# Kernel optimization log

Hardware: AMD Instinct MI355X
Metric: run time of the kernel (lower is better)

## Reference

```python
import jax, jax.numpy as jnp
import numpy as np

# ---- problem sizes ----
N_NEURONS = 1536
N_INPUTS = 768
BATCH = 32
T = 256
DT = 1.0  # ms per step
SURRGRAD_SCALE = 10.0

# ---- per-cell-type physiology (recurrent): 0=excitatory, 1=inhibitory ----
CELL_TAU_MEM = np.array([20.0, 10.0], np.float32)   # ms
CELL_THETA   = np.array([-50.0, -50.0], np.float32) # mV
CELL_URESET  = np.array([-65.0, -65.0], np.float32) # mV
CELL_EL      = np.array([-65.0, -65.0], np.float32) # mV
CELL_GL      = np.array([10.0, 10.0], np.float32)   # nS
CELL_TAUREF  = np.array([2.0, 1.0], np.float32)     # ms

# ---- synapse types: AMPA(pre=exc), NMDA(pre=exc), GABA_A(pre=inh) ----
SYN_CELL_ID   = np.array([0, 0, 1], np.int32)
SYN_TAU_RISE  = np.array([0.5, 2.0, 0.5], np.float32)
SYN_TAU_DECAY = np.array([2.0, 100.0, 5.0], np.float32)
SYN_EREV      = np.array([0.0, 0.0, -70.0], np.float32)
SYN_GBAR      = np.array([1.0, 0.5, 1.0], np.float32)

# ---- feedforward: single excitatory input type, single AMPA synapse ----
FF_TAU_RISE, FF_TAU_DECAY, FF_EREV, FF_GBAR = 0.5, 2.0, 0.0, 1.0


@jax.custom_vjp
def spike(v):
    # Heaviside spike with fast-sigmoid surrogate gradient
    return (v >= 0).astype(v.dtype)

def _spike_fwd(v):
    return spike(v), v

def _spike_bwd(v, g):
    return (g / (SURRGRAD_SCALE * jnp.abs(v) + 1.0) ** 2,)

spike.defvjp(_spike_fwd, _spike_bwd)


def setup_inputs() -> dict:
    key = jax.random.key(0)
    ks = jax.random.split(key, 6)
    input_spikes = (jax.random.uniform(ks[0], (BATCH, T, N_INPUTS)) < 0.05).astype(jnp.float32)
    weights = jax.random.normal(ks[1], (N_NEURONS, N_NEURONS), jnp.float32) * 0.05
    weights_FF = jax.random.normal(ks[2], (N_INPUTS, N_NEURONS), jnp.float32) * 0.05
    cell_type_indices = jax.random.randint(ks[3], (N_NEURONS,), 0, 2, jnp.int32)
    cell_type_indices_FF = jnp.zeros((N_INPUTS,), jnp.int32)
    scaling_factors = jax.random.uniform(ks[4], (2, 2), jnp.float32, 0.5, 1.5)
    scaling_factors_FF = jax.random.uniform(ks[5], (1, 2), jnp.float32, 0.5, 1.5)
    return {
        'input_spikes': input_spikes,
        'weights': weights,
        'weights_FF': weights_FF,
        'scaling_factors': scaling_factors,
        'scaling_factors_FF': scaling_factors_FF,
        'cell_type_indices': cell_type_indices,
        'cell_type_indices_FF': cell_type_indices_FF,
    }


def _simulate(input_spikes, weights, weights_FF, scaling_factors, scaling_factors_FF,
              cell_type_indices, cell_type_indices_FF):
    ct = cell_type_indices
    B = input_spikes.shape[0]

    # per-neuron physiology gathered by cell type
    tau_mem = jnp.asarray(CELL_TAU_MEM)[ct]
    theta = jnp.asarray(CELL_THETA)[ct]
    u_reset = jnp.asarray(CELL_URESET)[ct]
    e_l = jnp.asarray(CELL_EL)[ct]
    g_l = jnp.asarray(CELL_GL)[ct]
    ref_steps = jnp.asarray(CELL_TAUREF)[ct] / DT
    leak_coef = DT / (tau_mem * g_l)  # dt / C_m

    # effective weights: cell-type scaling + presynaptic synapse-type mask
    sf = scaling_factors[ct[:, None], ct[None, :]]            # (N, N)
    W = weights * sf
    pre_mask = (jnp.asarray(SYN_CELL_ID)[:, None] == ct[None, :]).astype(W.dtype)  # (S, N)
    Ws = W[None, :, :] * pre_mask[:, :, None]                  # (S, N, N)
    sfF = scaling_factors_FF[cell_type_indices_FF[:, None], ct[None, :]]
    WF = weights_FF * sfF                                      # (n_in, N)

    alpha_r = jnp.exp(-DT / jnp.asarray(SYN_TAU_RISE))[:, None, None]   # (S,1,1)
    alpha_d = jnp.exp(-DT / jnp.asarray(SYN_TAU_DECAY))[:, None, None]
    arF = jnp.exp(jnp.float32(-DT / FF_TAU_RISE))
    adF = jnp.exp(jnp.float32(-DT / FF_TAU_DECAY))
    gbar = jnp.asarray(SYN_GBAR)
    gbarE = jnp.asarray(SYN_GBAR * SYN_EREV)
    S = gbar.shape[0]

    U0 = jnp.broadcast_to(e_l, (B, N_NEURONS))
    carry0 = (U0,
              jnp.zeros((B, N_NEURONS), jnp.float32),       # previous spikes
              jnp.zeros((S, B, N_NEURONS), jnp.float32),    # x (rise)
              jnp.zeros((S, B, N_NEURONS), jnp.float32),    # g (decay)
              jnp.zeros((B, N_NEURONS), jnp.float32),       # x_FF
              jnp.zeros((B, N_NEURONS), jnp.float32),       # g_FF
              jnp.zeros((B, N_NEURONS), jnp.float32))       # refractory counter

    def step(carry, I_t):
        U, s_prev, x, g, xF, gF, ref = carry
        # dual-exponential conductance update per synapse type
        inp = jnp.einsum('bn,snm->sbm', s_prev, Ws)
        x = alpha_r * x + inp
        g = alpha_d * g + x
        xF = arF * xF + I_t @ WF
        gF = adF * gF + xF
        # conductance-based synaptic current: sum_s gbar_s * g_s * (E_s - U)
        gtot = jnp.einsum('s,sbn->bn', gbar, g) + FF_GBAR * gF
        gE = jnp.einsum('s,sbn->bn', gbarE, g) + (FF_GBAR * FF_EREV) * gF
        I_syn = gE - gtot * U
        # leaky membrane integration
        U_new = U + leak_coef * (g_l * (e_l - U) + I_syn)
        # refractory clamp
        in_ref = ref > 0
        U_new = jnp.where(in_ref, u_reset, U_new)
        ref = jnp.maximum(ref - 1.0, 0.0)
        # surrogate-gradient spike and reset
        s_new = spike(U_new - theta)
        U_out = jnp.where(s_new > 0, u_reset, U_new)
        ref = jnp.where(s_new > 0, ref_steps, ref)
        return (U_out, s_new, x, g, xF, gF, ref), (s_new, U_out)

    I_seq = jnp.transpose(input_spikes, (1, 0, 2))  # (T, B, n_in)
    _, (spk, volts) = jax.lax.scan(step, carry0, I_seq)
    return jnp.transpose(spk, (1, 0, 2)), jnp.transpose(volts, (1, 0, 2))


def reference(input_spikes, weights, weights_FF, scaling_factors, scaling_factors_FF,
              cell_type_indices, cell_type_indices_FF):
    return _simulate(input_spikes, weights, weights_FF, scaling_factors, scaling_factors_FF,
                     cell_type_indices, cell_type_indices_FF)
```

## Files before the change

kernel.cpp:

```cpp
#include <hip/hip_runtime.h>
#include <stdint.h>


__global__ __launch_bounds__(768) void snn_lif_kernel(
    const float* __restrict__ I,
    const float* __restrict__ W,
    const float* __restrict__ WF,
    const float* __restrict__ sf,
    const float* __restrict__ sfF,
    const int*   __restrict__ ct,
    float* __restrict__ out,
    uint64_t* __restrict__ recpub)
{
    const int tid = threadIdx.x;
    const int j   = blockIdx.x & 7;
    const int b   = blockIdx.x >> 3;
    const int wv  = tid >> 6;
    const int wl  = tid & 63;

    __shared__ float4   part0[2][12][48];
    __shared__ float4   part1[2][12][48];
    __shared__ float4   partF[2][12][48];
    __shared__ uint32_t ctm32_sh[48];

    for (int r = 0; r < 2; ++r) {
        int c = ct[r * 768 + tid];
        uint64_t bal = __ballot(c != 0);
        if (wl == 0) {
            ctm32_sh[r * 24 + wv * 2]     = (uint32_t)bal;
            ctm32_sh[r * 24 + wv * 2 + 1] = (uint32_t)(bal >> 32);
        }
    }
    __syncthreads();

    const int m = j * 192 + ((tid < 192) ? tid : 0);
    const int   myct = ct[m];
    const float s0m  = sf[myct];
    const float s1m  = sf[2 + myct];
    const float sFm  = sfF[myct];
    const float lc   = (myct == 0) ? (1.0f / 200.0f) : (1.0f / 100.0f);
    const float refsteps = (myct == 0) ? 2.0f : 1.0f;
    const float ar0 = expf(-1.0f / 0.5f),  ad0 = expf(-1.0f / 2.0f);
    const float ar1 = expf(-1.0f / 2.0f),  ad1 = expf(-1.0f / 100.0f);
    const float ar2 = expf(-1.0f / 0.5f),  ad2 = expf(-1.0f / 5.0f);
    const float arF = expf(-1.0f / 0.5f),  adF = expf(-1.0f / 2.0f);

    float U = -65.0f, refc = 0.0f;
    float x0 = 0, g0 = 0, x1 = 0, g1 = 0, x2 = 0, g2 = 0, xF = 0, gF = 0;

    const int  btbase  = b * 256;
    const bool gl      = (wl < 48);
    const uint32_t colbase = (uint32_t)(j * 192 + wl * 4);

    uint64_t fmask;
    {
        float iv = __builtin_nontemporal_load(
            &I[(uint32_t)btbase * 768u + (uint32_t)tid]);
        fmask = __ballot(iv > 0.5f);
    }

    for (int t = 0; t < 256; ++t) {
        float ivn = 0.0f;
        if (t < 255)
            ivn = __builtin_nontemporal_load(
                &I[(uint32_t)(btbase + t + 1) * 768u + (uint32_t)tid]);

        float4 a0 = make_float4(0.f, 0.f, 0.f, 0.f);
        float4 a1 = a0, aF = a0;

        {
            uint64_t mm = fmask;
            while (mm) {
                const int bit = __builtin_ctzll(mm);
                mm &= mm - 1;
                const uint32_t row = (uint32_t)(wv * 64 + bit);
                if (gl) {
                    const float4 w = *(const float4*)(WF + row * 1536u + colbase);
                    aF.x += w.x; aF.y += w.y; aF.z += w.z; aF.w += w.w;
                }
            }
        }

        if (t > 0) {
            uint32_t ready = 0;
            const uint32_t pbase = (uint32_t)(btbase + t - 1) * 48u + (uint32_t)(wv * 4);
            do {
                uint64_t pv = 0;
                if (wl < 4)
                    pv = __hip_atomic_load(&recpub[pbase + (uint32_t)wl],
                                           __ATOMIC_RELAXED, __HIP_MEMORY_SCOPE_AGENT);
                const uint32_t plo = (uint32_t)pv;
                const uint32_t phi = (uint32_t)(pv >> 32);
                #pragma unroll
                for (int k = 0; k < 4; ++k) {
                    if (ready & (1u << k)) continue;
                    const uint32_t tg = __builtin_amdgcn_readlane(phi, k);
                    if (tg != (uint32_t)t) continue;
                    ready |= 1u << k;
                    uint32_t bits = __builtin_amdgcn_readlane(plo, k);
                    const uint32_t word = (uint32_t)(wv * 4 + k);
                    const uint32_t cm = ctm32_sh[word];
                    while (bits) {
                        const int bit = __builtin_ctz(bits);
                        bits &= bits - 1;
                        const uint32_t row = word * 32u + (uint32_t)bit;
                        if (gl) {
                            const float4 w = *(const float4*)(W + row * 1536u + colbase);
                            if ((cm >> bit) & 1u) {
                                a1.x += w.x; a1.y += w.y; a1.z += w.z; a1.w += w.w;
                            } else {
                                a0.x += w.x; a0.y += w.y; a0.z += w.z; a0.w += w.w;
                            }
                        }
                    }
                }
            } while (ready != 0xFu);
        }

        const int buf = t & 1;
        if (gl) {
            part0[buf][wv][wl] = a0;
            part1[buf][wv][wl] = a1;
            partF[buf][wv][wl] = aF;
        }
        fmask = __ballot(ivn > 0.5f);
        __syncthreads();

        if (tid < 192) {
            const float* p0 = (const float*)&part0[buf][0][0];
            const float* p1 = (const float*)&part1[buf][0][0];
            const float* pF = (const float*)&partF[buf][0][0];
            float z0s = 0.f, z1s = 0.f, zFs = 0.f;
            #pragma unroll
            for (int k = 0; k < 12; ++k) {
                z0s += p0[k * 192 + tid];
                z1s += p1[k * 192 + tid];
                zFs += pF[k * 192 + tid];
            }
            z0s *= s0m; z1s *= s1m; zFs *= sFm;
            x0 = ar0 * x0 + z0s;  g0 = ad0 * g0 + x0;
            x1 = ar1 * x1 + z0s;  g1 = ad1 * g1 + x1;
            x2 = ar2 * x2 + z1s;  g2 = ad2 * g2 + x2;
            xF = arF * xF + zFs;  gF = adF * gF + xF;
            const float gtot = g0 + 0.5f * g1 + g2 + gF;
            const float gE   = -70.0f * g2;
            const float Isyn = gE - gtot * U;
            float Un = U + lc * (10.0f * (-65.0f - U) + Isyn);
            if (refc > 0.0f) Un = -65.0f;
            refc = fmaxf(refc - 1.0f, 0.0f);
            const bool s = (Un - (-50.0f)) >= 0.0f;
            const uint64_t bal = __ballot(s);
            if (wl == 0 || wl == 32) {
                const uint32_t half = (wl == 0) ? (uint32_t)bal : (uint32_t)(bal >> 32);
                const uint32_t word = (uint32_t)(j * 6 + wv * 2) + (wl == 32 ? 1u : 0u);
                const uint32_t widx = (uint32_t)(btbase + t) * 48u + word;
                const uint64_t v = ((uint64_t)(uint32_t)(t + 1) << 32) | half;
                __hip_atomic_store(&recpub[widx], v, __ATOMIC_RELAXED,
                                   __HIP_MEMORY_SCOPE_AGENT);
            }
            const float Uo = s ? -65.0f : Un;
            refc = s ? refsteps : refc;
            U = Uo;
            const uint32_t oidx = (uint32_t)(btbase + t) * 1536u + (uint32_t)m;
            __builtin_nontemporal_store(s ? 1.0f : 0.0f, &out[oidx]);
            __builtin_nontemporal_store(Uo, &out[12582912u + oidx]);
        }
    }
}

extern "C" void kernel_launch(void* const* d_in, const int* in_sizes, int n_in,
                              void* d_out, int out_size, void* d_ws, size_t ws_size,
                              hipStream_t stream) {
    const float* I   = (const float*)d_in[0];
    const float* W   = (const float*)d_in[1];
    const float* WF  = (const float*)d_in[2];
    const float* sf  = (const float*)d_in[3];
    const float* sfF = (const float*)d_in[4];
    const int*   ct  = (const int*)d_in[5];

    uint64_t* recpub = (uint64_t*)d_ws;

    snn_lif_kernel<<<dim3(256), dim3(768), 0, stream>>>(
        I, W, WF, sf, sfF, ct, (float*)d_out, recpub);
}
```

Before: 748.1 us.

## Overlap feedforward gather with recurrent wait and batch weight loads

Result: no change. 760.1 us (+1.6%).

```diff
diff --git a/kernel.cpp b/kernel.cpp
--- a/kernel.cpp
+++ b/kernel.cpp
@@ -1,6 +1,56 @@
 #include <hip/hip_runtime.h>
 #include <stdint.h>
 
+
+__device__ __forceinline__ uint64_t ld_g_sc0(const uint64_t* p) {
+    uint64_t v;
+    asm volatile("global_load_dwordx2 %0, %1, off sc0\n\t"
+                 "s_waitcnt vmcnt(0)"
+                 : "=v"(v) : "v"(p) : "memory");
+    return v;
+}
+
+__device__ __forceinline__ void st_g_sc0(uint64_t* p, uint64_t v) {
+    asm volatile("global_store_dwordx2 %0, %1, off sc0"
+                 :: "v"(p), "v"(v) : "memory");
+}
+
+__device__ __forceinline__ float4 ff_gather(const float* __restrict__ WF,
+                                            uint64_t mm, uint32_t rowbase,
+                                            uint32_t colbase) {
+    float4 acc = make_float4(0.f, 0.f, 0.f, 0.f);
+    while (mm) {
+        uint32_t q0 = 0, q1 = 0, q2 = 0, q3 = 0;
+        bool e1 = false, e2 = false, e3 = false;
+        { int bq = (int)__builtin_ctzll(mm); mm &= mm - 1; q0 = rowbase + (uint32_t)bq; }
+        if (mm) { int bq = (int)__builtin_ctzll(mm); mm &= mm - 1; q1 = rowbase + (uint32_t)bq; e1 = true; }
+        if (mm) { int bq = (int)__builtin_ctzll(mm); mm &= mm - 1; q2 = rowbase + (uint32_t)bq; e2 = true; }
+        if (mm) { int bq = (int)__builtin_ctzll(mm); mm &= mm - 1; q3 = rowbase + (uint32_t)bq; e3 = true; }
+        float4 u0, u1, u2, u3;
+        u0 = *(const float4*)(WF + q0 * 1536u + colbase);
+        if (e1) u1 = *(const float4*)(WF + q1 * 1536u + colbase);
+        if (e2) u2 = *(const float4*)(WF + q2 * 1536u + colbase);
+        if (e3) u3 = *(const float4*)(WF + q3 * 1536u + colbase);
+        acc.x += u0.x; acc.y += u0.y; acc.z += u0.z; acc.w += u0.w;
+        if (e1) { acc.x += u1.x; acc.y += u1.y; acc.z += u1.z; acc.w += u1.w; }
+        if (e2) { acc.x += u2.x; acc.y += u2.y; acc.z += u2.z; acc.w += u2.w; }
+        if (e3) { acc.x += u3.x; acc.y += u3.y; acc.z += u3.z; acc.w += u3.w; }
+    }
+    return acc;
+}
+
+#define POP_ROW(RV, CV, HV)                                                        \
+    {                                                                              \
+        HV = false;                                                                \
+        if (nb0)      { int _b = (int)__builtin_ctz(nb0); nb0 &= nb0 - 1;          \
+                        RV = wbase + (uint32_t)_b;        CV = (cm0 >> _b) & 1u; HV = true; } \
+        else if (nb1) { int _b = (int)__builtin_ctz(nb1); nb1 &= nb1 - 1;          \
+                        RV = wbase + 32u + (uint32_t)_b;  CV = (cm1 >> _b) & 1u; HV = true; } \
+        else if (nb2) { int _b = (int)__builtin_ctz(nb2); nb2 &= nb2 - 1;          \
+                        RV = wbase + 64u + (uint32_t)_b;  CV = (cm2 >> _b) & 1u; HV = true; } \
+        else if (nb3) { int _b = (int)__builtin_ctz(nb3); nb3 &= nb3 - 1;          \
+                        RV = wbase + 96u + (uint32_t)_b;  CV = (cm3 >> _b) & 1u; HV = true; } \
+    }
 
 __global__ __launch_bounds__(768) void snn_lif_kernel(
     const float* __restrict__ I,
@@ -10,13 +60,17 @@
     const float* __restrict__ sfF,
     const int*   __restrict__ ct,
     float* __restrict__ out,
-    uint64_t* __restrict__ recpub)
+    uint64_t* __restrict__ recpub,
+    uint64_t* __restrict__ recfast)
 {
+    __builtin_amdgcn_fence(__ATOMIC_ACQUIRE, "agent");
+
     const int tid = threadIdx.x;
-    const int j   = blockIdx.x & 7;
-    const int b   = blockIdx.x >> 3;
+    const int b   = blockIdx.x & 31;
+    const int j   = blockIdx.x >> 5;
     const int wv  = tid >> 6;
     const int wl  = tid & 63;
+    const bool havefast = (recfast != nullptr);
 
     __shared__ float4   part0[2][12][48];
     __shared__ float4   part1[2][12][48];
@@ -32,6 +86,11 @@
         }
     }
     __syncthreads();
+
+    const uint32_t cm0 = ctm32_sh[wv * 4 + 0];
+    const uint32_t cm1 = ctm32_sh[wv * 4 + 1];
+    const uint32_t cm2 = ctm32_sh[wv * 4 + 2];
+    const uint32_t cm3 = ctm32_sh[wv * 4 + 3];
 
     const int m = j * 192 + ((tid < 192) ? tid : 0);
     const int   myct = ct[m];
@@ -50,72 +109,84 @@
 
     const int  btbase  = b * 256;
     const bool gl      = (wl < 48);
-    const uint32_t colbase = (uint32_t)(j * 192 + wl * 4);
-
-    uint64_t fmask;
+    const uint32_t colbase = (uint32_t)(j * 192) + (uint32_t)((wl < 48 ? wl : 47) * 4);
+    const uint32_t wbase   = (uint32_t)(wv * 128);
+    const uint32_t ffbase  = (uint32_t)(wv * 64);
+
+    float4 aF;
     {
         float iv = __builtin_nontemporal_load(
             &I[(uint32_t)btbase * 768u + (uint32_t)tid]);
-        fmask = __ballot(iv > 0.5f);
+        uint64_t f0 = __ballot(iv > 0.5f);
+        aF = ff_gather(WF, f0, ffbase, colbase);
     }
 
     for (int t = 0; t < 256; ++t) {
+        float4 a0 = make_float4(0.f, 0.f, 0.f, 0.f);
+        float4 a1 = a0;
+
+        if (t > 0) {
+            uint32_t ready = 0;
+            const uint32_t pbase = (uint32_t)(btbase + t - 1) * 48u + (uint32_t)(wv * 4);
+            uint32_t nb0 = 0, nb1 = 0, nb2 = 0, nb3 = 0;
+            int it = 0;
+            do {
+                uint64_t pv = 0;
+                if (wl < 4) {
+                    if (havefast && ((it & 1) == 0))
+                        pv = ld_g_sc0(&recfast[pbase + (uint32_t)wl]);
+                    else
+                        pv = __hip_atomic_load(&recpub[pbase + (uint32_t)wl],
+                                               __ATOMIC_RELAXED, __HIP_MEMORY_SCOPE_AGENT);
+                }
+                ++it;
+                const uint32_t plo = (uint32_t)pv;
+                const uint32_t phi = (uint32_t)(pv >> 32);
+                if (!(ready & 1u) && (uint32_t)__builtin_amdgcn_readlane(phi, 0) == (uint32_t)t) {
+                    ready |= 1u; nb0 = (uint32_t)__builtin_amdgcn_readlane(plo, 0);
+                }
+                if (!(ready & 2u) && (uint32_t)__builtin_amdgcn_readlane(phi, 1) == (uint32_t)t) {
+                    ready |= 2u; nb1 = (uint32_t)__builtin_amdgcn_readlane(plo, 1);
+                }
+                if (!(ready & 4u) && (uint32_t)__builtin_amdgcn_readlane(phi, 2) == (uint32_t)t) {
+                    ready |= 4u; nb2 = (uint32_t)__builtin_amdgcn_readlane(plo, 2);
+                }
+                if (!(ready & 8u) && (uint32_t)__builtin_amdgcn_readlane(phi, 3) == (uint32_t)t) {
+                    ready |= 8u; nb3 = (uint32_t)__builtin_amdgcn_readlane(plo, 3);
+                }
+                while (nb0 | nb1 | nb2 | nb3) {
+                    uint32_t r0 = 0, r1 = 0, r2 = 0, r3 = 0;
+                    uint32_t c0 = 0, c1 = 0, c2 = 0, c3 = 0;
+                    bool h0 = false, h1 = false, h2 = false, h3 = false;
+                    POP_ROW(r0, c0, h0); POP_ROW(r1, c1, h1);
+                    POP_ROW(r2, c2, h2); POP_ROW(r3, c3, h3);
+                    float4 w0, w1, w2, w3;
+                    w0 = *(const float4*)(W + r0 * 1536u + colbase);
+                    if (h1) w1 = *(const float4*)(W + r1 * 1536u + colbase);
+                    if (h2) w2 = *(const float4*)(W + r2 * 1536u + colbase);
+                    if (h3) w3 = *(const float4*)(W + r3 * 1536u + colbase);
+                    if (c0) { a1.x += w0.x; a1.y += w0.y; a1.z += w0.z; a1.w += w0.w; }
+                    else    { a0.x += w0.x; a0.y += w0.y; a0.z += w0.z; a0.w += w0.w; }
+                    if (h1) {
+                        if (c1) { a1.x += w1.x; a1.y += w1.y; a1.z += w1.z; a1.w += w1.w; }
+                        else    { a0.x += w1.x; a0.y += w1.y; a0.z += w1.z; a0.w += w1.w; }
+                    }
+                    if (h2) {
+                        if (c2) { a1.x += w2.x; a1.y += w2.y; a1.z += w2.z; a1.w += w2.w; }
+                        else    { a0.x += w2.x; a0.y += w2.y; a0.z += w2.z; a0.w += w2.w; }
+                    }
+                    if (h3) {
+                        if (c3) { a1.x += w3.x; a1.y += w3.y; a1.z += w3.z; a1.w += w3.w; }
+                        else    { a0.x += w3.x; a0.y += w3.y; a0.z += w3.z; a0.w += w3.w; }
+                    }
+                }
+            } while (ready != 0xFu);
+        }
+
         float ivn = 0.0f;
         if (t < 255)
             ivn = __builtin_nontemporal_load(
                 &I[(uint32_t)(btbase + t + 1) * 768u + (uint32_t)tid]);
-
-        float4 a0 = make_float4(0.f, 0.f, 0.f, 0.f);
-        float4 a1 = a0, aF = a0;
-
-        {
-            uint64_t mm = fmask;
-            while (mm) {
-                const int bit = __builtin_ctzll(mm);
-                mm &= mm - 1;
-                const uint32_t row = (uint32_t)(wv * 64 + bit);
-                if (gl) {
-                    const float4 w = *(const float4*)(WF + row * 1536u + colbase);
-                    aF.x += w.x; aF.y += w.y; aF.z += w.z; aF.w += w.w;
-                }
-            }
-        }
-
-        if (t > 0) {
-            uint32_t ready = 0;
-            const uint32_t pbase = (uint32_t)(btbase + t - 1) * 48u + (uint32_t)(wv * 4);
-            do {
-                uint64_t pv = 0;
-                if (wl < 4)
-                    pv = __hip_atomic_load(&recpub[pbase + (uint32_t)wl],
-                                           __ATOMIC_RELAXED, __HIP_MEMORY_SCOPE_AGENT);
-                const uint32_t plo = (uint32_t)pv;
-                const uint32_t phi = (uint32_t)(pv >> 32);
-                #pragma unroll
-                for (int k = 0; k < 4; ++k) {
-                    if (ready & (1u << k)) continue;
-                    const uint32_t tg = __builtin_amdgcn_readlane(phi, k);
-                    if (tg != (uint32_t)t) continue;
-                    ready |= 1u << k;
-                    uint32_t bits = __builtin_amdgcn_readlane(plo, k);
-                    const uint32_t word = (uint32_t)(wv * 4 + k);
-                    const uint32_t cm = ctm32_sh[word];
-                    while (bits) {
-                        const int bit = __builtin_ctz(bits);
-                        bits &= bits - 1;
-                        const uint32_t row = word * 32u + (uint32_t)bit;
-                        if (gl) {
-                            const float4 w = *(const float4*)(W + row * 1536u + colbase);
-                            if ((cm >> bit) & 1u) {
-                                a1.x += w.x; a1.y += w.y; a1.z += w.z; a1.w += w.w;
-                            } else {
-                                a0.x += w.x; a0.y += w.y; a0.z += w.z; a0.w += w.w;
-                            }
-                        }
-                    }
-                }
-            } while (ready != 0xFu);
-        }
 
         const int buf = t & 1;
         if (gl) {
@@ -123,7 +194,6 @@
             part1[buf][wv][wl] = a1;
             partF[buf][wv][wl] = aF;
         }
-        fmask = __ballot(ivn > 0.5f);
         __syncthreads();
 
         if (tid < 192) {
@@ -157,6 +227,7 @@
                 const uint64_t v = ((uint64_t)(uint32_t)(t + 1) << 32) | half;
                 __hip_atomic_store(&recpub[widx], v, __ATOMIC_RELAXED,
                                    __HIP_MEMORY_SCOPE_AGENT);
+                if (havefast) st_g_sc0(&recfast[widx], v);
             }
             const float Uo = s ? -65.0f : Un;
             refc = s ? refsteps : refc;
@@ -164,6 +235,11 @@
             const uint32_t oidx = (uint32_t)(btbase + t) * 1536u + (uint32_t)m;
             __builtin_nontemporal_store(s ? 1.0f : 0.0f, &out[oidx]);
             __builtin_nontemporal_store(Uo, &out[12582912u + oidx]);
+        }
+
+        {
+            uint64_t fmask = __ballot(ivn > 0.5f);
+            aF = ff_gather(WF, fmask, ffbase, colbase);
         }
     }
 }
@@ -178,8 +254,11 @@
     const float* sfF = (const float*)d_in[4];
     const int*   ct  = (const int*)d_in[5];
 
-    uint64_t* recpub = (uint64_t*)d_ws;
+    const size_t SZ = 32ull * 256ull * 48ull * 8ull;
+    uint64_t* recpub  = (uint64_t*)d_ws;
+    uint64_t* recfast = (ws_size >= 2 * SZ)
+                        ? (uint64_t*)((char*)d_ws + SZ) : nullptr;
 
     snn_lif_kernel<<<dim3(256), dim3(768), 0, stream>>>(
-        I, W, WF, sf, sfF, ct, (float*)d_out, recpub);
-}
+        I, W, WF, sf, sfF, ct, (float*)d_out, recpub, recfast);
+}
```

## Halve block count with 384 neurons per block and all lanes active

Applied to the files above, without the earlier changes.

Result: slower. 935.8 us (+25.1%).

```diff
diff --git a/kernel.cpp b/kernel.cpp
--- a/kernel.cpp
+++ b/kernel.cpp
@@ -1,6 +1,8 @@
 #include <hip/hip_runtime.h>
 #include <stdint.h>
 
+
+#define ATOMIC_LD(p) __hip_atomic_load((p), __ATOMIC_RELAXED, __HIP_MEMORY_SCOPE_AGENT)
 
 __global__ __launch_bounds__(768) void snn_lif_kernel(
     const float* __restrict__ I,
@@ -13,14 +15,12 @@
     uint64_t* __restrict__ recpub)
 {
     const int tid = threadIdx.x;
-    const int j   = blockIdx.x & 7;
-    const int b   = blockIdx.x >> 3;
+    const int j   = blockIdx.x & 3;
+    const int b   = blockIdx.x >> 2;
     const int wv  = tid >> 6;
     const int wl  = tid & 63;
 
-    __shared__ float4   part0[2][12][48];
-    __shared__ float4   part1[2][12][48];
-    __shared__ float4   partF[2][12][48];
+    __shared__ float    partf[2][12][3][384];
     __shared__ uint32_t ctm32_sh[48];
 
     for (int r = 0; r < 2; ++r) {
@@ -33,12 +33,16 @@
     }
     __syncthreads();
 
-    const int m = j * 192 + ((tid < 192) ? tid : 0);
+    uint32_t cmw[4];
+    #pragma unroll
+    for (int k = 0; k < 4; ++k) cmw[k] = ctm32_sh[wv * 4 + k];
+
+    const int   m    = j * 384 + wv * 32 + (wl & 31);
     const int   myct = ct[m];
     const float s0m  = sf[myct];
     const float s1m  = sf[2 + myct];
     const float sFm  = sfF[myct];
-    const float lc   = (myct == 0) ? (1.0f / 200.0f) : (1.0f / 100.0f);
+    const float lcoef = (myct == 0) ? (1.0f / 200.0f) : (1.0f / 100.0f);
     const float refsteps = (myct == 0) ? 2.0f : 1.0f;
     const float ar0 = expf(-1.0f / 0.5f),  ad0 = expf(-1.0f / 2.0f);
     const float ar1 = expf(-1.0f / 2.0f),  ad1 = expf(-1.0f / 100.0f);
@@ -48,9 +52,9 @@
     float U = -65.0f, refc = 0.0f;
     float x0 = 0, g0 = 0, x1 = 0, g1 = 0, x2 = 0, g2 = 0, xF = 0, gF = 0;
 
-    const int  btbase  = b * 256;
-    const bool gl      = (wl < 48);
-    const uint32_t colbase = (uint32_t)(j * 192 + wl * 4);
+    const int btbase = b * 256;
+    const uint32_t c4 = (uint32_t)(j * 384) + (uint32_t)(wl * 4);
+    const uint32_t c2 = (uint32_t)(j * 384) + 256u + (uint32_t)(wl * 2);
 
     uint64_t fmask;
     {
@@ -60,101 +64,114 @@
     }
 
     for (int t = 0; t < 256; ++t) {
+        const uint32_t pbase = (uint32_t)(btbase + t - 1) * 48u + (uint32_t)(wv * 4);
+        uint64_t pv = 0;
+        if (t > 0 && wl < 4)
+            pv = ATOMIC_LD(&recpub[pbase + (uint32_t)wl]);
+
         float ivn = 0.0f;
         if (t < 255)
             ivn = __builtin_nontemporal_load(
                 &I[(uint32_t)(btbase + t + 1) * 768u + (uint32_t)tid]);
 
-        float4 a0 = make_float4(0.f, 0.f, 0.f, 0.f);
-        float4 a1 = a0, aF = a0;
+        float4 a04 = make_float4(0.f, 0.f, 0.f, 0.f), a14 = a04, aF4 = a04;
+        float2 a02 = make_float2(0.f, 0.f),           a12 = a02, aF2 = a02;
 
         {
             uint64_t mm = fmask;
             while (mm) {
                 const int bit = __builtin_ctzll(mm);
                 mm &= mm - 1;
-                const uint32_t row = (uint32_t)(wv * 64 + bit);
-                if (gl) {
-                    const float4 w = *(const float4*)(WF + row * 1536u + colbase);
-                    aF.x += w.x; aF.y += w.y; aF.z += w.z; aF.w += w.w;
-                }
+                const float* rp = WF + (size_t)(wv * 64 + bit) * 1536u;
+                const float4 w4 = *(const float4*)(rp + c4);
+                const float2 w2 = *(const float2*)(rp + c2);
+                aF4.x += w4.x; aF4.y += w4.y; aF4.z += w4.z; aF4.w += w4.w;
+                aF2.x += w2.x; aF2.y += w2.y;
             }
         }
 
         if (t > 0) {
             uint32_t ready = 0;
-            const uint32_t pbase = (uint32_t)(btbase + t - 1) * 48u + (uint32_t)(wv * 4);
-            do {
-                uint64_t pv = 0;
-                if (wl < 4)
-                    pv = __hip_atomic_load(&recpub[pbase + (uint32_t)wl],
-                                           __ATOMIC_RELAXED, __HIP_MEMORY_SCOPE_AGENT);
+            for (;;) {
                 const uint32_t plo = (uint32_t)pv;
                 const uint32_t phi = (uint32_t)(pv >> 32);
                 #pragma unroll
                 for (int k = 0; k < 4; ++k) {
                     if (ready & (1u << k)) continue;
-                    const uint32_t tg = __builtin_amdgcn_readlane(phi, k);
-                    if (tg != (uint32_t)t) continue;
+                    if ((uint32_t)__builtin_amdgcn_readlane(phi, k) != (uint32_t)t)
+                        continue;
                     ready |= 1u << k;
-                    uint32_t bits = __builtin_amdgcn_readlane(plo, k);
+                    uint32_t bits = (uint32_t)__builtin_amdgcn_readlane(plo, k);
+                    const uint32_t cm   = cmw[k];
                     const uint32_t word = (uint32_t)(wv * 4 + k);
-                    const uint32_t cm = ctm32_sh[word];
                     while (bits) {
                         const int bit = __builtin_ctz(bits);
                         bits &= bits - 1;
-                        const uint32_t row = word * 32u + (uint32_t)bit;
-                        if (gl) {
-                            const float4 w = *(const float4*)(W + row * 1536u + colbase);
-                            if ((cm >> bit) & 1u) {
-                                a1.x += w.x; a1.y += w.y; a1.z += w.z; a1.w += w.w;
-                            } else {
-                                a0.x += w.x; a0.y += w.y; a0.z += w.z; a0.w += w.w;
-                            }
+                        const float* rp = W + (size_t)(word * 32u + (uint32_t)bit) * 1536u;
+                        const float4 w4 = *(const float4*)(rp + c4);
+                        const float2 w2 = *(const float2*)(rp + c2);
+                        if ((cm >> bit) & 1u) {
+                            a14.x += w4.x; a14.y += w4.y; a14.z += w4.z; a14.w += w4.w;
+                            a12.x += w2.x; a12.y += w2.y;
+                        } else {
+                            a04.x += w4.x; a04.y += w4.y; a04.z += w4.z; a04.w += w4.w;
+                            a02.x += w2.x; a02.y += w2.y;
                         }
                     }
                 }
-            } while (ready != 0xFu);
+                if (ready == 0xFu) break;
+                pv = 0;
+                if (wl < 4)
+                    pv = ATOMIC_LD(&recpub[pbase + (uint32_t)wl]);
+            }
         }
 
         const int buf = t & 1;
-        if (gl) {
-            part0[buf][wv][wl] = a0;
-            part1[buf][wv][wl] = a1;
-            partF[buf][wv][wl] = aF;
+        {
+            float* b0 = &partf[buf][wv][0][0];
+            float* b1 = &partf[buf][wv][1][0];
+            float* b2 = &partf[buf][wv][2][0];
+            ((float4*)b0)[wl] = a04;  *(float2*)(b0 + 256 + wl * 2) = a02;
+            ((float4*)b1)[wl] = a14;  *(float2*)(b1 + 256 + wl * 2) = a12;
+            ((float4*)b2)[wl] = aF4;  *(float2*)(b2 + 256 + wl * 2) = aF2;
         }
         fmask = __ballot(ivn > 0.5f);
         __syncthreads();
 
-        if (tid < 192) {
-            const float* p0 = (const float*)&part0[buf][0][0];
-            const float* p1 = (const float*)&part1[buf][0][0];
-            const float* pF = (const float*)&partF[buf][0][0];
-            float z0s = 0.f, z1s = 0.f, zFs = 0.f;
+        {
+            const int h6 = (wl >> 5) * 6;
+            const int lc = wv * 32 + (wl & 31);
+            const float* pf = &partf[buf][0][0][0];
+            float z0 = 0.f, z1 = 0.f, zF = 0.f;
             #pragma unroll
-            for (int k = 0; k < 12; ++k) {
-                z0s += p0[k * 192 + tid];
-                z1s += p1[k * 192 + tid];
-                zFs += pF[k * 192 + tid];
-            }
-            z0s *= s0m; z1s *= s1m; zFs *= sFm;
-            x0 = ar0 * x0 + z0s;  g0 = ad0 * g0 + x0;
-            x1 = ar1 * x1 + z0s;  g1 = ad1 * g1 + x1;
-            x2 = ar2 * x2 + z1s;  g2 = ad2 * g2 + x2;
-            xF = arF * xF + zFs;  gF = adF * gF + xF;
+            for (int i = 0; i < 6; ++i) {
+                const int w = h6 + i;
+                z0 += pf[(w * 3 + 0) * 384 + lc];
+                z1 += pf[(w * 3 + 1) * 384 + lc];
+                zF += pf[(w * 3 + 2) * 384 + lc];
+            }
+            z0 += __shfl_xor(z0, 32);
+            z1 += __shfl_xor(z1, 32);
+            zF += __shfl_xor(zF, 32);
+            z0 *= s0m; z1 *= s1m; zF *= sFm;
+
+            x0 = ar0 * x0 + z0;  g0 = ad0 * g0 + x0;
+            x1 = ar1 * x1 + z0;  g1 = ad1 * g1 + x1;
+            x2 = ar2 * x2 + z1;  g2 = ad2 * g2 + x2;
+            xF = arF * xF + zF;  gF = adF * gF + xF;
             const float gtot = g0 + 0.5f * g1 + g2 + gF;
             const float gE   = -70.0f * g2;
             const float Isyn = gE - gtot * U;
-            float Un = U + lc * (10.0f * (-65.0f - U) + Isyn);
+            float Un = U + lcoef * (10.0f * (-65.0f - U) + Isyn);
             if (refc > 0.0f) Un = -65.0f;
             refc = fmaxf(refc - 1.0f, 0.0f);
             const bool s = (Un - (-50.0f)) >= 0.0f;
+
             const uint64_t bal = __ballot(s);
-            if (wl == 0 || wl == 32) {
-                const uint32_t half = (wl == 0) ? (uint32_t)bal : (uint32_t)(bal >> 32);
-                const uint32_t word = (uint32_t)(j * 6 + wv * 2) + (wl == 32 ? 1u : 0u);
-                const uint32_t widx = (uint32_t)(btbase + t) * 48u + word;
-                const uint64_t v = ((uint64_t)(uint32_t)(t + 1) << 32) | half;
+            if (wl == 0) {
+                const uint32_t widx = (uint32_t)(btbase + t) * 48u
+                                      + (uint32_t)(j * 12 + wv);
+                const uint64_t v = ((uint64_t)(uint32_t)(t + 1) << 32) | (uint32_t)bal;
                 __hip_atomic_store(&recpub[widx], v, __ATOMIC_RELAXED,
                                    __HIP_MEMORY_SCOPE_AGENT);
             }
@@ -162,8 +179,10 @@
             refc = s ? refsteps : refc;
             U = Uo;
             const uint32_t oidx = (uint32_t)(btbase + t) * 1536u + (uint32_t)m;
-            __builtin_nontemporal_store(s ? 1.0f : 0.0f, &out[oidx]);
-            __builtin_nontemporal_store(Uo, &out[12582912u + oidx]);
+            if (wl < 32)
+                __builtin_nontemporal_store(s ? 1.0f : 0.0f, &out[oidx]);
+            else
+                __builtin_nontemporal_store(Uo, &out[12582912u + oidx]);
         }
     }
 }
@@ -180,6 +199,6 @@
 
     uint64_t* recpub = (uint64_t*)d_ws;
 
-    snn_lif_kernel<<<dim3(256), dim3(768), 0, stream>>>(
+    snn_lif_kernel<<<dim3(128), dim3(768), 0, stream>>>(
         I, W, WF, sf, sfF, ct, (float*)d_out, recpub);
 }
```

## Load-balance spike row accumulation across waves via shared-memory work queue

Applied to the files above, without the earlier changes.

Measured after the change: 1.277 ms. 70.7% more time.

```diff
diff --git a/kernel.cpp b/kernel.cpp
--- a/kernel.cpp
+++ b/kernel.cpp
@@ -1,6 +1,21 @@
 #include <hip/hip_runtime.h>
 #include <stdint.h>
 
+
+#define ATOMIC_LD(p) __hip_atomic_load((p), __ATOMIC_RELAXED, __HIP_MEMORY_SCOPE_AGENT)
+#define LDS_LD(p)    __hip_atomic_load((p), __ATOMIC_RELAXED, __HIP_MEMORY_SCOPE_WORKGROUP)
+#define LDS_ST(p, v) __hip_atomic_store((p), (v), __ATOMIC_RELAXED, __HIP_MEMORY_SCOPE_WORKGROUP)
+
+#define ACCW(CLS, W4) do {                                                     \
+    if ((CLS) == 0u)      { a0.x += (W4).x; a0.y += (W4).y;                    \
+                            a0.z += (W4).z; a0.w += (W4).w; }                  \
+    else if ((CLS) == 1u) { a1.x += (W4).x; a1.y += (W4).y;                    \
+                            a1.z += (W4).z; a1.w += (W4).w; }                  \
+    else                  { aF.x += (W4).x; aF.y += (W4).y;                    \
+                            aF.z += (W4).z; aF.w += (W4).w; }                  \
+} while (0)
+
+#define QCAP 2308
 
 __global__ __launch_bounds__(768) void snn_lif_kernel(
     const float* __restrict__ I,
@@ -22,6 +37,18 @@
     __shared__ float4   part1[2][12][48];
     __shared__ float4   partF[2][12][48];
     __shared__ uint32_t ctm32_sh[48];
+    __shared__ uint16_t queue_sh[2][QCAP];
+    __shared__ int      tail_sh[2], head_sh[2], wdone_sh[2];
+
+    for (int i = tid; i < QCAP; i += 768) {
+        queue_sh[0][i] = 0xFFFFu;
+        queue_sh[1][i] = 0xFFFFu;
+    }
+    if (tid == 0) {
+        tail_sh[0] = tail_sh[1] = 0;
+        head_sh[0] = head_sh[1] = 0;
+        wdone_sh[0] = wdone_sh[1] = 0;
+    }
 
     for (int r = 0; r < 2; ++r) {
         int c = ct[r * 768 + tid];
@@ -32,6 +59,10 @@
         }
     }
     __syncthreads();
+
+    uint32_t cmw[4];
+    #pragma unroll
+    for (int k = 0; k < 4; ++k) cmw[k] = ctm32_sh[wv * 4 + k];
 
     const int m = j * 192 + ((tid < 192) ? tid : 0);
     const int   myct = ct[m];
@@ -48,9 +79,9 @@
     float U = -65.0f, refc = 0.0f;
     float x0 = 0, g0 = 0, x1 = 0, g1 = 0, x2 = 0, g2 = 0, xF = 0, gF = 0;
 
-    const int  btbase  = b * 256;
-    const bool gl      = (wl < 48);
-    const uint32_t colbase = (uint32_t)(j * 192 + wl * 4);
+    const int  btbase = b * 256;
+    const bool gl     = (wl < 48);
+    const uint32_t colbase = (uint32_t)(j * 192) + (uint32_t)((wl < 48 ? wl : 47) * 4);
 
     uint64_t fmask;
     {
@@ -60,64 +91,145 @@
     }
 
     for (int t = 0; t < 256; ++t) {
+        const int buf = t & 1;
+        uint16_t*                 qq = &queue_sh[buf][0];
+        volatile const uint16_t*  qv = &queue_sh[buf][0];
+
+        const uint32_t pbase = (uint32_t)(btbase + t - 1) * 48u + (uint32_t)(wv * 4);
+        uint64_t pv0 = 0;
+        if (t > 0 && wl < 4)
+            pv0 = ATOMIC_LD(&recpub[pbase + (uint32_t)wl]);
+
         float ivn = 0.0f;
         if (t < 255)
             ivn = __builtin_nontemporal_load(
                 &I[(uint32_t)(btbase + t + 1) * 768u + (uint32_t)tid]);
 
+        if (fmask) {
+            const int cnt = __builtin_popcountll(fmask);
+            int b0 = 0;
+            if (wl == 0) b0 = atomicAdd(&tail_sh[buf], cnt);
+            b0 = __shfl(b0, 0);
+            if ((fmask >> (uint32_t)wl) & 1ull) {
+                const uint32_t pos = (uint32_t)__builtin_popcountll(
+                    fmask & ((1ull << (uint32_t)wl) - 1ull));
+                qq[b0 + (int)pos] = (uint16_t)(0x2000u | (uint32_t)(wv * 64 + wl));
+            }
+        }
+
         float4 a0 = make_float4(0.f, 0.f, 0.f, 0.f);
         float4 a1 = a0, aF = a0;
 
-        {
-            uint64_t mm = fmask;
-            while (mm) {
-                const int bit = __builtin_ctzll(mm);
-                mm &= mm - 1;
-                const uint32_t row = (uint32_t)(wv * 64 + bit);
+        uint32_t ready  = (t > 0) ? 0u : 0xFu;
+        bool     counted = false;
+        bool     havepv  = (t > 0);
+        uint64_t pvcur   = pv0;
+
+        for (;;) {
+            if (ready != 0xFu && !havepv) {
+                pvcur = 0;
+                if (wl < 4) pvcur = ATOMIC_LD(&recpub[pbase + (uint32_t)wl]);
+                havepv = true;
+            }
+            int got = 0, gbase = 0, term = 0;
+            if (wl == 0) {
+                const int wd = LDS_LD(&wdone_sh[buf]);
+                __threadfence_block();
+                int hd = LDS_LD(&head_sh[buf]);
+                int tl = LDS_LD(&tail_sh[buf]);
+                while (hd < tl) {
+                    const int want = (hd + 4 < tl) ? hd + 4 : tl;
+                    const int old  = atomicCAS(&head_sh[buf], hd, want);
+                    if (old == hd) { got = want - hd; gbase = hd; break; }
+                    hd = old;
+                    tl = LDS_LD(&tail_sh[buf]);
+                }
+                if (got == 0 && wd == 12 && hd >= tl) term = 1;
+            }
+            got = __shfl(got, 0);
+            if (got) {
+                gbase = __shfl(gbase, 0);
+                uint32_t e0, e1, e2, e3;
+                for (;;) {
+                    uint32_t ev = 0xFFFFu;
+                    if (wl < 4) ev = qv[gbase + wl];
+                    e0 = (uint32_t)__builtin_amdgcn_readlane(ev, 0);
+                    e1 = (uint32_t)__builtin_amdgcn_readlane(ev, 1);
+                    e2 = (uint32_t)__builtin_amdgcn_readlane(ev, 2);
+                    e3 = (uint32_t)__builtin_amdgcn_readlane(ev, 3);
+                    bool ok = (e0 != 0xFFFFu);
+                    if (got > 1 && e1 == 0xFFFFu) ok = false;
+                    if (got > 2 && e2 == 0xFFFFu) ok = false;
+                    if (got > 3 && e3 == 0xFFFFu) ok = false;
+                    if (ok) break;
+                }
                 if (gl) {
-                    const float4 w = *(const float4*)(WF + row * 1536u + colbase);
-                    aF.x += w.x; aF.y += w.y; aF.z += w.z; aF.w += w.w;
+                    const uint32_t r0 = e0 & 0xFFFu, c0 = e0 >> 12;
+                    const float4 w0 = *(const float4*)(
+                        ((c0 == 2u) ? WF : W) + (size_t)r0 * 1536u + colbase);
+                    float4 w1, w2, w3;
+                    uint32_t c1 = 0, c2 = 0, c3 = 0;
+                    if (got > 1) {
+                        const uint32_t r1 = e1 & 0xFFFu; c1 = e1 >> 12;
+                        w1 = *(const float4*)(
+                            ((c1 == 2u) ? WF : W) + (size_t)r1 * 1536u + colbase);
+                    }
+                    if (got > 2) {
+                        const uint32_t r2 = e2 & 0xFFFu; c2 = e2 >> 12;
+                        w2 = *(const float4*)(
+                            ((c2 == 2u) ? WF : W) + (size_t)r2 * 1536u + colbase);
+                    }
+                    if (got > 3) {
+                        const uint32_t r3 = e3 & 0xFFFu; c3 = e3 >> 12;
+                        w3 = *(const float4*)(
+                            ((c3 == 2u) ? WF : W) + (size_t)r3 * 1536u + colbase);
+                    }
+                    ACCW(c0, w0);
+                    if (got > 1) ACCW(c1, w1);
+                    if (got > 2) ACCW(c2, w2);
+                    if (got > 3) ACCW(c3, w3);
                 }
             }
-        }
-
-        if (t > 0) {
-            uint32_t ready = 0;
-            const uint32_t pbase = (uint32_t)(btbase + t - 1) * 48u + (uint32_t)(wv * 4);
-            do {
-                uint64_t pv = 0;
-                if (wl < 4)
-                    pv = __hip_atomic_load(&recpub[pbase + (uint32_t)wl],
-                                           __ATOMIC_RELAXED, __HIP_MEMORY_SCOPE_AGENT);
-                const uint32_t plo = (uint32_t)pv;
-                const uint32_t phi = (uint32_t)(pv >> 32);
+            if (ready != 0xFu && havepv) {
+                const uint32_t plo = (uint32_t)pvcur;
+                const uint32_t phi = (uint32_t)(pvcur >> 32);
                 #pragma unroll
                 for (int k = 0; k < 4; ++k) {
                     if (ready & (1u << k)) continue;
-                    const uint32_t tg = __builtin_amdgcn_readlane(phi, k);
-                    if (tg != (uint32_t)t) continue;
+                    if ((uint32_t)__builtin_amdgcn_readlane(phi, k) != (uint32_t)t)
+                        continue;
                     ready |= 1u << k;
-                    uint32_t bits = __builtin_amdgcn_readlane(plo, k);
-                    const uint32_t word = (uint32_t)(wv * 4 + k);
-                    const uint32_t cm = ctm32_sh[word];
-                    while (bits) {
-                        const int bit = __builtin_ctz(bits);
-                        bits &= bits - 1;
-                        const uint32_t row = word * 32u + (uint32_t)bit;
-                        if (gl) {
-                            const float4 w = *(const float4*)(W + row * 1536u + colbase);
-                            if ((cm >> bit) & 1u) {
-                                a1.x += w.x; a1.y += w.y; a1.z += w.z; a1.w += w.w;
-                            } else {
-                                a0.x += w.x; a0.y += w.y; a0.z += w.z; a0.w += w.w;
-                            }
+                    const uint32_t bits = (uint32_t)__builtin_amdgcn_readlane(plo, k);
+                    if (bits) {
+                        const int cnt = __builtin_popcount(bits);
+                        int b0 = 0;
+                        if (wl == 0) b0 = atomicAdd(&tail_sh[buf], cnt);
+                        b0 = __shfl(b0, 0);
+                        if (wl < 32 && ((bits >> (uint32_t)wl) & 1u)) {
+                            const uint32_t pos = __builtin_popcount(
+                                bits & ((1u << (uint32_t)wl) - 1u));
+                            const uint32_t cls = (cmw[k] >> (uint32_t)wl) & 1u;
+                            qq[b0 + (int)pos] = (uint16_t)(
+                                (cls << 12) |
+                                ((uint32_t)(wv * 4 + k) * 32u + (uint32_t)wl));
                         }
                     }
                 }
-            } while (ready != 0xFu);
-        }
-
-        const int buf = t & 1;
+                havepv = false;
+            }
+            if (ready == 0xFu && !counted) {
+                __threadfence_block();
+                if (wl == 0) atomicAdd(&wdone_sh[buf], 1);
+                counted = true;
+            }
+            if (!got) {
+                term = __shfl(term, 0);
+                if (term) break;
+            }
+        }
+
+        const int tfin = LDS_LD(&tail_sh[buf]);
+
         if (gl) {
             part0[buf][wv][wl] = a0;
             part1[buf][wv][wl] = a1;
@@ -165,6 +277,13 @@
             __builtin_nontemporal_store(s ? 1.0f : 0.0f, &out[oidx]);
             __builtin_nontemporal_store(Uo, &out[12582912u + oidx]);
         }
+
+        for (int i = tid; i < tfin; i += 768) qq[i] = 0xFFFFu;
+        if (tid == 0) {
+            LDS_ST(&tail_sh[buf], 0);
+            LDS_ST(&head_sh[buf], 0);
+            LDS_ST(&wdone_sh[buf], 0);
+        }
     }
 }
 
```
